# Kernel optimization log

Hardware: AMD Instinct MI355X
Metric: run time of the kernel (lower is better)

## Reference

```python
import jax, jax.numpy as jnp
import numpy as np

EPS = 1e-12  # matches torch F.normalize default eps


def _l2_normalize(x):
    # torch.nn.functional.normalize: x / max(||x||, eps)
    n = jnp.sqrt(jnp.sum(x * x, axis=-1, keepdims=True))
    return x / jnp.maximum(n, EPS)


def setup_inputs() -> dict:
    key = jax.random.key(0)
    kq, kk, kv = jax.random.split(key, 3)
    B, KD, VD, N = 256, 128, 128, 500000
    return {
        "query": jax.random.normal(kq, (B, KD), dtype=jnp.float32),
        "keys": jax.random.normal(kk, (N, KD), dtype=jnp.float32),
        "values": jax.random.normal(kv, (N, VD), dtype=jnp.float32),
        "k": 8,
    }


def reference(query, keys, values, k):
    # Cosine similarity: normalize both sides, dense matmul.
    q_norm = _l2_normalize(query)            # [B, KD]
    k_norm = _l2_normalize(keys)             # [N, KD]
    sim = jnp.matmul(q_norm, k_norm.T)       # [B, N]
    scores, indices = jax.lax.top_k(sim, k)  # [B, k] each
    slots = values[indices]                  # gather -> [B, k, VD]
    return slots, scores
```

## Files before the change

### kernel.cpp

```cpp
#include <hip/hip_runtime.h>
#include <math.h>

#define B     256
#define KD    128
#define VD    128
#define TOPK  8
#define NBK   512
#define QG    4
#define KB    16

typedef __attribute__((ext_vector_type(8))) short bf16x8;
typedef __attribute__((ext_vector_type(4))) float f32x4;

__device__ __forceinline__ bool gt_si(float a, int ai, float b, int bi) {
    return (a > b) || (a == b && ai < bi);
}

__device__ __forceinline__ float bf16lo_f(unsigned int p) { return __uint_as_float(p << 16); }
__device__ __forceinline__ float bf16hi_f(unsigned int p) { return __uint_as_float(p & 0xffff0000u); }

#define SPLIT_PAIR(x0, x1, o1, o2, o3)                                         \
    {                                                                          \
        unsigned int p1_, p2_, p3_;                                            \
        float xx0_ = (x0), xx1_ = (x1);                                        \
        asm("v_cvt_pk_bf16_f32 %0, %1, %2" : "=v"(p1_) : "v"(xx0_), "v"(xx1_));\
        float r0_ = xx0_ - bf16lo_f(p1_);                                      \
        float r1_ = xx1_ - bf16hi_f(p1_);                                      \
        asm("v_cvt_pk_bf16_f32 %0, %1, %2" : "=v"(p2_) : "v"(r0_), "v"(r1_));  \
        float t0_ = r0_ - bf16lo_f(p2_);                                       \
        float t1_ = r1_ - bf16hi_f(p2_);                                       \
        asm("v_cvt_pk_bf16_f32 %0, %1, %2" : "=v"(p3_) : "v"(t0_), "v"(t1_));  \
        o1 = p1_; o2 = p2_; o3 = p3_;                                          \
    }

__global__ __launch_bounds__(64) void k_prep_q(const float* __restrict__ q,
                                               unsigned int* __restrict__ qb) {
    const int qt   = blockIdx.x;
    const int l    = threadIdx.x;
    const int qcol = l & 15;
    const int ck   = l >> 4;
    const int qrow = qt * 16 + qcol;

    const float4* src = (const float4*)(q + (size_t)qrow * KD + ck * 32);
    float4 v[8];
    float ss = 0.f;
#pragma unroll
    for (int i = 0; i < 8; ++i) {
        v[i] = src[i];
        ss += v[i].x * v[i].x + v[i].y * v[i].y + v[i].z * v[i].z + v[i].w * v[i].w;
    }
    ss += __shfl_xor(ss, 16);
    ss += __shfl_xor(ss, 32);
    const float inv = 1.0f / fmaxf(sqrtf(ss), 1e-12f);

    float x[32];
#pragma unroll
    for (int i = 0; i < 8; ++i) {
        x[4 * i + 0] = v[i].x * inv;
        x[4 * i + 1] = v[i].y * inv;
        x[4 * i + 2] = v[i].z * inv;
        x[4 * i + 3] = v[i].w * inv;
    }

#pragma unroll
    for (int h = 0; h < 4; ++h) {
        unsigned int u1[4], u2[4], u3[4];
#pragma unroll
        for (int p = 0; p < 4; ++p) {
            SPLIT_PAIR(x[h * 8 + 2 * p], x[h * 8 + 2 * p + 1], u1[p], u2[p], u3[p]);
        }
        const int lam = h * 16 + qcol;
        *(uint4*)&qb[((((size_t)0 * 16 + qt) * 4 + ck) * 64 + lam) * 4] = make_uint4(u1[0], u1[1], u1[2], u1[3]);
        *(uint4*)&qb[((((size_t)1 * 16 + qt) * 4 + ck) * 64 + lam) * 4] = make_uint4(u2[0], u2[1], u2[2], u2[3]);
        *(uint4*)&qb[((((size_t)2 * 16 + qt) * 4 + ck) * 64 + lam) * 4] = make_uint4(u3[0], u3[1], u3[2], u3[3]);
    }
}

__global__ __launch_bounds__(256, 2) void k_cand(const float* __restrict__ keys,
                                                 const unsigned int* __restrict__ qb,
                                                 float* __restrict__ cand_s,
                                                 int* __restrict__ cand_i,
                                                 int N, int chunk) {
    __shared__ __align__(16) unsigned short lk[3 * 16 * 136];

    const int t  = threadIdx.x;
    const int l  = t & 63;
    const int w  = t >> 6;
    const int bx = blockIdx.x;
    const int qg = blockIdx.y;
    const int qt = qg * 4 + w;

    const int base = bx * chunk;
    const int nend = min(N, base + chunk);

    bf16x8 bq[3][4];
#pragma unroll
    for (int term = 0; term < 3; ++term)
#pragma unroll
        for (int ks = 0; ks < 4; ++ks) {
            const uint4 u = *(const uint4*)&qb[((((size_t)term * 16 + qt) * 4 + ks) * 64 + l) * 4];
            bq[term][ks] = *(const bf16x8*)&u;
        }

    float s[TOPK];
    int   id[TOPK];
#pragma unroll
    for (int j = 0; j < TOPK; ++j) { s[j] = -1e30f; id[j] = 0; }

    const int srow = t >> 4;
    const int sseg = t & 15;
    const int ro   = (l & 15) * 136 + (l >> 4) * 8;

    for (int sb = base; sb < nend; sb += KB) {
        const int row = sb + srow;
        float4 a, c;
        if (row < nend) {
            const float4* kr = (const float4*)(keys + (size_t)row * KD + sseg * 8);
            a = kr[0];
            c = kr[1];
        } else {
            a = make_float4(0.f, 0.f, 0.f, 0.f);
            c = a;
        }
        float ss = a.x * a.x + a.y * a.y + a.z * a.z + a.w * a.w
                 + c.x * c.x + c.y * c.y + c.z * c.z + c.w * c.w;
#pragma unroll
        for (int m = 8; m >= 1; m >>= 1) ss += __shfl_xor(ss, m);
        const float inv = 1.0f / fmaxf(sqrtf(ss), 1e-12f);
        const float x0 = a.x * inv, x1 = a.y * inv, x2 = a.z * inv, x3 = a.w * inv;
        const float x4 = c.x * inv, x5 = c.y * inv, x6 = c.z * inv, x7 = c.w * inv;

        unsigned int u1[4], u2[4], u3[4];
        SPLIT_PAIR(x0, x1, u1[0], u2[0], u3[0]);
        SPLIT_PAIR(x2, x3, u1[1], u2[1], u3[1]);
        SPLIT_PAIR(x4, x5, u1[2], u2[2], u3[2]);
        SPLIT_PAIR(x6, x7, u1[3], u2[3], u3[3]);

        const int wo = srow * 136 + sseg * 8;
        *(uint4*)&lk[0 * 2176 + wo] = make_uint4(u1[0], u1[1], u1[2], u1[3]);
        *(uint4*)&lk[1 * 2176 + wo] = make_uint4(u2[0], u2[1], u2[2], u2[3]);
        *(uint4*)&lk[2 * 2176 + wo] = make_uint4(u3[0], u3[1], u3[2], u3[3]);
        __syncthreads();

        bf16x8 ak[3][4];
#pragma unroll
        for (int term = 0; term < 3; ++term)
#pragma unroll
            for (int ks = 0; ks < 4; ++ks)
                ak[term][ks] = *(const bf16x8*)&lk[term * 2176 + ro + ks * 32];
        __syncthreads();

        f32x4 acc0 = {0.f, 0.f, 0.f, 0.f};
        f32x4 acc1 = {0.f, 0.f, 0.f, 0.f};
        f32x4 acc2 = {0.f, 0.f, 0.f, 0.f};
        f32x4 acc3 = {0.f, 0.f, 0.f, 0.f};
#define PRD(ta, tb)                                                                     \
        acc0 = __builtin_amdgcn_mfma_f32_16x16x32_bf16(ak[ta][0], bq[tb][0], acc0, 0, 0, 0); \
        acc1 = __builtin_amdgcn_mfma_f32_16x16x32_bf16(ak[ta][1], bq[tb][1], acc1, 0, 0, 0); \
        acc2 = __builtin_amdgcn_mfma_f32_16x16x32_bf16(ak[ta][2], bq[tb][2], acc2, 0, 0, 0); \
        acc3 = __builtin_amdgcn_mfma_f32_16x16x32_bf16(ak[ta][3], bq[tb][3], acc3, 0, 0, 0);
        PRD(0, 2) PRD(2, 0) PRD(1, 1) PRD(0, 1) PRD(1, 0) PRD(0, 0)
#undef PRD
        f32x4 sim4 = (acc0 + acc1) + (acc2 + acc3);

        const int kb0 = sb + (l >> 4) * 4;
#pragma unroll
        for (int r = 0; r < 4; ++r) {
            const int kidx = kb0 + r;
            float sim = sim4[r];
            sim = (kidx < nend) ? sim : -1e30f;
            if (sim > s[TOPK - 1]) {
                s[TOPK - 1]  = sim;
                id[TOPK - 1] = kidx;
#pragma unroll
                for (int u = TOPK - 1; u >= 1; --u) {
                    const bool sw = s[u] > s[u - 1];
                    if (sw) {
                        float ts = s[u]; s[u] = s[u - 1]; s[u - 1] = ts;
                        int   ti = id[u]; id[u] = id[u - 1]; id[u - 1] = ti;
                    }
                }
            }
        }
    }

#pragma unroll
    for (int m = 16; m <= 32; m <<= 1) {
        float bs[TOPK]; int bi[TOPK];
#pragma unroll
        for (int j = 0; j < TOPK; ++j) {
            bs[j] = __shfl_xor(s[j], m);
            bi[j] = __shfl_xor(id[j], m);
        }
        float ms[TOPK]; int mi[TOPK];
#pragma unroll
        for (int j = 0; j < TOPK; ++j) {
            const float av = s[j];            const int ai = id[j];
            const float bv = bs[TOPK - 1 - j]; const int b2 = bi[TOPK - 1 - j];
            const bool g = gt_si(av, ai, bv, b2);
            ms[j] = g ? av : bv;
            mi[j] = g ? ai : b2;
        }
#define CAS_(x, y)                                                     \
        { if (!gt_si(ms[x], mi[x], ms[y], mi[y])) {                    \
              float tv = ms[x]; ms[x] = ms[y]; ms[y] = tv;             \
              int   ti = mi[x]; mi[x] = mi[y]; mi[y] = ti; } }
        CAS_(0, 4); CAS_(1, 5); CAS_(2, 6); CAS_(3, 7);
        CAS_(0, 2); CAS_(1, 3); CAS_(4, 6); CAS_(5, 7);
        CAS_(0, 1); CAS_(2, 3); CAS_(4, 5); CAS_(6, 7);
#undef CAS_
#pragma unroll
        for (int j = 0; j < TOPK; ++j) { s[j] = ms[j]; id[j] = mi[j]; }
    }

    if ((l >> 4) == 0) {
        const int q = qt * 16 + (l & 15);
        float* os = cand_s + ((size_t)bx * B + q) * TOPK;
        int*   oi = cand_i + ((size_t)bx * B + q) * TOPK;
#pragma unroll
        for (int j = 0; j < TOPK; ++j) { os[j] = s[j]; oi[j] = id[j]; }
    }
}

__global__ __launch_bounds__(64) void k_merge(const float* __restrict__ cand_s,
                                              const int* __restrict__ cand_i,
                                              const float* __restrict__ values,
                                              float* __restrict__ out_slots,
                                              float* __restrict__ out_scores) {
    const int q    = blockIdx.x;
    const int lane = threadIdx.x;

    float s[TOPK];
    int   id[TOPK];
#pragma unroll
    for (int j = 0; j < TOPK; ++j) { s[j] = -1e30f; id[j] = -1; }

    for (int b = lane; b < NBK; b += 64) {
        const float* cs = cand_s + ((size_t)b * B + q) * TOPK;
        const int*   ci = cand_i + ((size_t)b * B + q) * TOPK;
#pragma unroll
        for (int j = 0; j < TOPK; ++j) {
            const float v  = cs[j];
            const int   vi = ci[j];
            if (gt_si(v, vi, s[TOPK - 1], id[TOPK - 1])) {
                s[TOPK - 1]  = v;
                id[TOPK - 1] = vi;
#pragma unroll
                for (int u = TOPK - 1; u >= 1; --u) {
                    if (gt_si(s[u], id[u], s[u - 1], id[u - 1])) {
                        float ts = s[u]; s[u] = s[u - 1]; s[u - 1] = ts;
                        int   ti = id[u]; id[u] = id[u - 1]; id[u - 1] = ti;
                    }
                }
            }
        }
    }

#pragma unroll
    for (int m = 1; m <= 32; m <<= 1) {
        float bs[TOPK]; int bi[TOPK];
#pragma unroll
        for (int j = 0; j < TOPK; ++j) {
            bs[j] = __shfl_xor(s[j], m);
            bi[j] = __shfl_xor(id[j], m);
        }
        float ms[TOPK]; int mi[TOPK];
#pragma unroll
        for (int j = 0; j < TOPK; ++j) {
            const float av = s[j];            const int ai = id[j];
            const float bv = bs[TOPK - 1 - j]; const int b2 = bi[TOPK - 1 - j];
            const bool g = gt_si(av, ai, bv, b2);
            ms[j] = g ? av : bv;
            mi[j] = g ? ai : b2;
        }
#define CAS_(x, y)                                                     \
        { if (!gt_si(ms[x], mi[x], ms[y], mi[y])) {                    \
              float tv = ms[x]; ms[x] = ms[y]; ms[y] = tv;             \
              int   ti = mi[x]; mi[x] = mi[y]; mi[y] = ti; } }
        CAS_(0, 4); CAS_(1, 5); CAS_(2, 6); CAS_(3, 7);
        CAS_(0, 2); CAS_(1, 3); CAS_(4, 6); CAS_(5, 7);
        CAS_(0, 1); CAS_(2, 3); CAS_(4, 5); CAS_(6, 7);
#undef CAS_
#pragma unroll
        for (int j = 0; j < TOPK; ++j) { s[j] = ms[j]; id[j] = mi[j]; }
    }

    if (lane == 0) {
#pragma unroll
        for (int j = 0; j < TOPK; ++j) out_scores[(size_t)q * TOPK + j] = s[j];
    }

#pragma unroll
    for (int j = 0; j < TOPK; ++j) {
        const int row = id[j];
        const float2* src = (const float2*)(values + (size_t)row * VD);
        float2 v = src[lane];
        ((float2*)(out_slots + ((size_t)q * TOPK + j) * VD))[lane] = v;
    }
}

extern "C" void kernel_launch(void* const* d_in, const int* in_sizes, int n_in,
                              void* d_out, int out_size, void* d_ws, size_t ws_size,
                              hipStream_t stream) {
    const float* q      = (const float*)d_in[0];
    const float* keys   = (const float*)d_in[1];
    const float* values = (const float*)d_in[2];
    const int N = in_sizes[1] / KD;

    float* out_slots  = (float*)d_out;
    float* out_scores = out_slots + (size_t)B * TOPK * VD;

    unsigned int* qbuf = (unsigned int*)d_ws;
    float* cand_s = (float*)(qbuf + 49152);
    int*   cand_i = (int*)(cand_s + (size_t)NBK * B * TOPK);

    const int chunk = (N + NBK - 1) / NBK;

    k_prep_q<<<16, 64, 0, stream>>>(q, qbuf);
    dim3 grid(NBK, QG);
    k_cand<<<grid, 256, 0, stream>>>(keys, qbuf, cand_s, cand_i, N, chunk);
    k_merge<<<B, 64, 0, stream>>>(cand_s, cand_i, values, out_slots, out_scores);
}
```

Measured before the change: 736.8 us.

## Precompute normalized bf16x3 key tiles once and stream them into MFMA

Adds a k_prep_k pass that normalizes every key once and writes its three-term bf16 split, already in the MFMA operand layout, to workspace. The candidate kernel then loads those fragments directly from global memory, with no per-tile normalization, LDS staging or barriers. This removes the conversion work the old kernel repeated for each of the four query groups. Block indices are remapped so the four query groups sharing a key chunk run close together and can reuse it from cache, and the candidate buffer is transposed to query-major for the merge. The cost is writing and rereading a precomputed key buffer about 1.5x the size of the fp32 keys, and the new path needs a large workspace, falling back to the old kernel when it is too small.

```diff
diff --git a/kernel.cpp b/kernel.cpp
--- a/kernel.cpp
+++ b/kernel.cpp
@@ -33,6 +33,11 @@
         o1 = p1_; o2 = p2_; o3 = p3_;                                          \
     }
 
+__device__ __forceinline__ void decode_bq(int flat, int& bx, int& qg) {
+    bx = ((flat >> 5) << 3) | (flat & 7);
+    qg = (flat >> 3) & 3;
+}
+
 __global__ __launch_bounds__(64) void k_prep_q(const float* __restrict__ q,
                                                unsigned int* __restrict__ qb) {
     const int qt   = blockIdx.x;
@@ -76,79 +81,95 @@
     }
 }
 
-__global__ __launch_bounds__(256, 2) void k_cand(const float* __restrict__ keys,
-                                                 const unsigned int* __restrict__ qb,
-                                                 float* __restrict__ cand_s,
-                                                 int* __restrict__ cand_i,
-                                                 int N, int chunk) {
-    __shared__ __align__(16) unsigned short lk[3 * 16 * 136];
-
-    const int t  = threadIdx.x;
-    const int l  = t & 63;
-    const int w  = t >> 6;
-    const int bx = blockIdx.x;
-    const int qg = blockIdx.y;
-    const int qt = qg * 4 + w;
-
-    const int base = bx * chunk;
-    const int nend = min(N, base + chunk);
-
-    bf16x8 bq[3][4];
-#pragma unroll
-    for (int term = 0; term < 3; ++term)
-#pragma unroll
-        for (int ks = 0; ks < 4; ++ks) {
-            const uint4 u = *(const uint4*)&qb[((((size_t)term * 16 + qt) * 4 + ks) * 64 + l) * 4];
-            bq[term][ks] = *(const bf16x8*)&u;
-        }
-
-    float s[TOPK];
-    int   id[TOPK];
-#pragma unroll
-    for (int j = 0; j < TOPK; ++j) { s[j] = -1e30f; id[j] = 0; }
-
-    const int srow = t >> 4;
-    const int sseg = t & 15;
-    const int ro   = (l & 15) * 136 + (l >> 4) * 8;
-
-    for (int sb = base; sb < nend; sb += KB) {
-        const int row = sb + srow;
-        float4 a, c;
-        if (row < nend) {
-            const float4* kr = (const float4*)(keys + (size_t)row * KD + sseg * 8);
-            a = kr[0];
-            c = kr[1];
+__global__ __launch_bounds__(256, 2) void k_prep_k(const float* __restrict__ keys,
+                                                   uint4* __restrict__ kb,
+                                                   int N, int ntiles) {
+    const int w    = threadIdx.x >> 6;
+    const int l    = threadIdx.x & 63;
+    const int tile = blockIdx.x * 4 + w;
+    if (tile >= ntiles) return;
+
+    const int row = tile * 16 + (l & 15);
+    const int h   = l >> 4;
+
+    float4 va[4], vb[4];
+    float ss = 0.f;
+#pragma unroll
+    for (int ks = 0; ks < 4; ++ks) {
+        if (row < N) {
+            const float4* src = (const float4*)(keys + (size_t)row * KD + ks * 32 + h * 8);
+            va[ks] = src[0];
+            vb[ks] = src[1];
         } else {
-            a = make_float4(0.f, 0.f, 0.f, 0.f);
-            c = a;
-        }
-        float ss = a.x * a.x + a.y * a.y + a.z * a.z + a.w * a.w
-                 + c.x * c.x + c.y * c.y + c.z * c.z + c.w * c.w;
-#pragma unroll
-        for (int m = 8; m >= 1; m >>= 1) ss += __shfl_xor(ss, m);
-        const float inv = 1.0f / fmaxf(sqrtf(ss), 1e-12f);
-        const float x0 = a.x * inv, x1 = a.y * inv, x2 = a.z * inv, x3 = a.w * inv;
-        const float x4 = c.x * inv, x5 = c.y * inv, x6 = c.z * inv, x7 = c.w * inv;
-
+            va[ks] = make_float4(0.f, 0.f, 0.f, 0.f);
+            vb[ks] = va[ks];
+        }
+        ss += va[ks].x * va[ks].x + va[ks].y * va[ks].y + va[ks].z * va[ks].z + va[ks].w * va[ks].w
+            + vb[ks].x * vb[ks].x + vb[ks].y * vb[ks].y + vb[ks].z * vb[ks].z + vb[ks].w * vb[ks].w;
+    }
+    ss += __shfl_xor(ss, 16);
+    ss += __shfl_xor(ss, 32);
+    const float inv = 1.0f / fmaxf(sqrtf(ss), 1e-12f);
+
+#pragma unroll
+    for (int ks = 0; ks < 4; ++ks) {
+        const float x0 = va[ks].x * inv, x1 = va[ks].y * inv;
+        const float x2 = va[ks].z * inv, x3 = va[ks].w * inv;
+        const float x4 = vb[ks].x * inv, x5 = vb[ks].y * inv;
+        const float x6 = vb[ks].z * inv, x7 = vb[ks].w * inv;
         unsigned int u1[4], u2[4], u3[4];
         SPLIT_PAIR(x0, x1, u1[0], u2[0], u3[0]);
         SPLIT_PAIR(x2, x3, u1[1], u2[1], u3[1]);
         SPLIT_PAIR(x4, x5, u1[2], u2[2], u3[2]);
         SPLIT_PAIR(x6, x7, u1[3], u2[3], u3[3]);
-
-        const int wo = srow * 136 + sseg * 8;
-        *(uint4*)&lk[0 * 2176 + wo] = make_uint4(u1[0], u1[1], u1[2], u1[3]);
-        *(uint4*)&lk[1 * 2176 + wo] = make_uint4(u2[0], u2[1], u2[2], u2[3]);
-        *(uint4*)&lk[2 * 2176 + wo] = make_uint4(u3[0], u3[1], u3[2], u3[3]);
-        __syncthreads();
-
+        const size_t tb = (size_t)tile * 12;
+        kb[(tb + 0 * 4 + ks) * 64 + l] = make_uint4(u1[0], u1[1], u1[2], u1[3]);
+        kb[(tb + 1 * 4 + ks) * 64 + l] = make_uint4(u2[0], u2[1], u2[2], u2[3]);
+        kb[(tb + 2 * 4 + ks) * 64 + l] = make_uint4(u3[0], u3[1], u3[2], u3[3]);
+    }
+}
+
+__global__ __launch_bounds__(256, 2) void k_cand_fast(const uint4* __restrict__ kb,
+                                                      const unsigned int* __restrict__ qb,
+                                                      float* __restrict__ cand_s,
+                                                      int* __restrict__ cand_i,
+                                                      int N, int ntiles, int tiles_per_bx) {
+    const int t = threadIdx.x;
+    const int l = t & 63;
+    const int w = t >> 6;
+    int bx, qg;
+    decode_bq(blockIdx.x, bx, qg);
+    const int qt = qg * 4 + w;
+
+    const int t0 = bx * tiles_per_bx;
+    const int t1 = min(ntiles, t0 + tiles_per_bx);
+
+    bf16x8 bq[3][4];
+#pragma unroll
+    for (int term = 0; term < 3; ++term)
+#pragma unroll
+        for (int ks = 0; ks < 4; ++ks) {
+            const uint4 u = *(const uint4*)&qb[((((size_t)term * 16 + qt) * 4 + ks) * 64 + l) * 4];
+            bq[term][ks] = *(const bf16x8*)&u;
+        }
+
+    float s[TOPK];
+    int   id[TOPK];
+#pragma unroll
+    for (int j = 0; j < TOPK; ++j) { s[j] = -1e30f; id[j] = 0; }
+
+    const uint4* kbl = kb + l;
+
+    for (int tile = t0; tile < t1; ++tile) {
+        const uint4* kt = kbl + (size_t)tile * 12 * 64;
         bf16x8 ak[3][4];
 #pragma unroll
         for (int term = 0; term < 3; ++term)
 #pragma unroll
-            for (int ks = 0; ks < 4; ++ks)
-                ak[term][ks] = *(const bf16x8*)&lk[term * 2176 + ro + ks * 32];
-        __syncthreads();
+            for (int ks = 0; ks < 4; ++ks) {
+                const uint4 u = kt[(term * 4 + ks) * 64];
+                ak[term][ks] = *(const bf16x8*)&u;
+            }
 
         f32x4 acc0 = {0.f, 0.f, 0.f, 0.f};
         f32x4 acc1 = {0.f, 0.f, 0.f, 0.f};
@@ -163,12 +184,12 @@
 #undef PRD
         f32x4 sim4 = (acc0 + acc1) + (acc2 + acc3);
 
-        const int kb0 = sb + (l >> 4) * 4;
+        const int kb0 = tile * 16 + (l >> 4) * 4;
 #pragma unroll
         for (int r = 0; r < 4; ++r) {
             const int kidx = kb0 + r;
             float sim = sim4[r];
-            sim = (kidx < nend) ? sim : -1e30f;
+            sim = (kidx < N) ? sim : -1e30f;
             if (sim > s[TOPK - 1]) {
                 s[TOPK - 1]  = sim;
                 id[TOPK - 1] = kidx;
@@ -215,39 +236,113 @@
 
     if ((l >> 4) == 0) {
         const int q = qt * 16 + (l & 15);
-        float* os = cand_s + ((size_t)bx * B + q) * TOPK;
-        int*   oi = cand_i + ((size_t)bx * B + q) * TOPK;
+        float* os = cand_s + ((size_t)q * NBK + bx) * TOPK;
+        int*   oi = cand_i + ((size_t)q * NBK + bx) * TOPK;
 #pragma unroll
         for (int j = 0; j < TOPK; ++j) { os[j] = s[j]; oi[j] = id[j]; }
     }
 }
 
-__global__ __launch_bounds__(64) void k_merge(const float* __restrict__ cand_s,
-                                              const int* __restrict__ cand_i,
-                                              const float* __restrict__ values,
-                                              float* __restrict__ out_slots,
-                                              float* __restrict__ out_scores) {
-    const int q    = blockIdx.x;
-    const int lane = threadIdx.x;
+__global__ __launch_bounds__(256, 2) void k_cand_slow(const float* __restrict__ keys,
+                                                      const unsigned int* __restrict__ qb,
+                                                      float* __restrict__ cand_s,
+                                                      int* __restrict__ cand_i,
+                                                      int N, int chunk) {
+    __shared__ __align__(16) unsigned short lk[3 * 16 * 136];
+
+    const int t = threadIdx.x;
+    const int l = t & 63;
+    const int w = t >> 6;
+    int bx, qg;
+    decode_bq(blockIdx.x, bx, qg);
+    const int qt = qg * 4 + w;
+
+    const int base = bx * chunk;
+    const int nend = min(N, base + chunk);
+
+    bf16x8 bq[3][4];
+#pragma unroll
+    for (int term = 0; term < 3; ++term)
+#pragma unroll
+        for (int ks = 0; ks < 4; ++ks) {
+            const uint4 u = *(const uint4*)&qb[((((size_t)term * 16 + qt) * 4 + ks) * 64 + l) * 4];
+            bq[term][ks] = *(const bf16x8*)&u;
+        }
 
     float s[TOPK];
     int   id[TOPK];
 #pragma unroll
-    for (int j = 0; j < TOPK; ++j) { s[j] = -1e30f; id[j] = -1; }
-
-    for (int b = lane; b < NBK; b += 64) {
-        const float* cs = cand_s + ((size_t)b * B + q) * TOPK;
-        const int*   ci = cand_i + ((size_t)b * B + q) * TOPK;
-#pragma unroll
-        for (int j = 0; j < TOPK; ++j) {
-            const float v  = cs[j];
-            const int   vi = ci[j];
-            if (gt_si(v, vi, s[TOPK - 1], id[TOPK - 1])) {
-                s[TOPK - 1]  = v;
-                id[TOPK - 1] = vi;
+    for (int j = 0; j < TOPK; ++j) { s[j] = -1e30f; id[j] = 0; }
+
+    const int srow = t >> 4;
+    const int sseg = t & 15;
+    const int ro   = (l & 15) * 136 + (l >> 4) * 8;
+
+    for (int sb = base; sb < nend; sb += KB) {
+        const int row = sb + srow;
+        float4 a, c;
+        if (row < nend) {
+            const float4* kr = (const float4*)(keys + (size_t)row * KD + sseg * 8);
+            a = kr[0];
+            c = kr[1];
+        } else {
+            a = make_float4(0.f, 0.f, 0.f, 0.f);
+            c = a;
+        }
+        float ss = a.x * a.x + a.y * a.y + a.z * a.z + a.w * a.w
+                 + c.x * c.x + c.y * c.y + c.z * c.z + c.w * c.w;
+#pragma unroll
+        for (int m = 8; m >= 1; m >>= 1) ss += __shfl_xor(ss, m);
+        const float inv = 1.0f / fmaxf(sqrtf(ss), 1e-12f);
+        const float x0 = a.x * inv, x1 = a.y * inv, x2 = a.z * inv, x3 = a.w * inv;
+        const float x4 = c.x * inv, x5 = c.y * inv, x6 = c.z * inv, x7 = c.w * inv;
+
+        unsigned int u1[4], u2[4], u3[4];
+        SPLIT_PAIR(x0, x1, u1[0], u2[0], u3[0]);
+        SPLIT_PAIR(x2, x3, u1[1], u2[1], u3[1]);
+        SPLIT_PAIR(x4, x5, u1[2], u2[2], u3[2]);
+        SPLIT_PAIR(x6, x7, u1[3], u2[3], u3[3]);
+
+        const int wo = srow * 136 + sseg * 8;
+        *(uint4*)&lk[0 * 2176 + wo] = make_uint4(u1[0], u1[1], u1[2], u1[3]);
+        *(uint4*)&lk[1 * 2176 + wo] = make_uint4(u2[0], u2[1], u2[2], u2[3]);
+        *(uint4*)&lk[2 * 2176 + wo] = make_uint4(u3[0], u3[1], u3[2], u3[3]);
+        __syncthreads();
+
+        bf16x8 ak[3][4];
+#pragma unroll
+        for (int term = 0; term < 3; ++term)
+#pragma unroll
+            for (int ks = 0; ks < 4; ++ks)
+                ak[term][ks] = *(const bf16x8*)&lk[term * 2176 + ro + ks * 32];
+        __syncthreads();
+
+        f32x4 acc0 = {0.f, 0.f, 0.f, 0.f};
+        f32x4 acc1 = {0.f, 0.f, 0.f, 0.f};
+        f32x4 acc2 = {0.f, 0.f, 0.f, 0.f};
+        f32x4 acc3 = {0.f, 0.f, 0.f, 0.f};
+#define PRD(ta, tb)                                                                     \
+        acc0 = __builtin_amdgcn_mfma_f32_16x16x32_bf16(ak[ta][0], bq[tb][0], acc0, 0, 0, 0); \
+        acc1 = __builtin_amdgcn_mfma_f32_16x16x32_bf16(ak[ta][1], bq[tb][1], acc1, 0, 0, 0); \
+        acc2 = __builtin_amdgcn_mfma_f32_16x16x32_bf16(ak[ta][2], bq[tb][2], acc2, 0, 0, 0); \
+        acc3 = __builtin_amdgcn_mfma_f32_16x16x32_bf16(ak[ta][3], bq[tb][3], acc3, 0, 0, 0);
+        PRD(0, 2) PRD(2, 0) PRD(1, 1) PRD(0, 1) PRD(1, 0) PRD(0, 0)
+#undef PRD
+        f32x4 sim4 = (acc0 + acc1) + (acc2 + acc3);
+
+        const int kb0 = sb + (l >> 4) * 4;
+#pragma unroll
+        for (int r = 0; r < 4; ++r) {
+            const int kidx = kb0 + r;
+            float sim = sim4[r];
+            sim = (kidx < nend) ? sim : -1e30f;
+            if (sim > s[TOPK - 1]) {
+                s[TOPK - 1]  = sim;
+                id[TOPK - 1] = kidx;
 #pragma unroll
                 for (int u = TOPK - 1; u >= 1; --u) {
-                    if (gt_si(s[u], id[u], s[u - 1], id[u - 1])) {
+                    const bool sw = s[u] > s[u - 1];
+                    if (sw) {
                         float ts = s[u]; s[u] = s[u - 1]; s[u - 1] = ts;
                         int   ti = id[u]; id[u] = id[u - 1]; id[u - 1] = ti;
                     }
@@ -257,7 +352,7 @@
     }
 
 #pragma unroll
-    for (int m = 1; m <= 32; m <<= 1) {
+    for (int m = 16; m <= 32; m <<= 1) {
         float bs[TOPK]; int bi[TOPK];
 #pragma unroll
         for (int j = 0; j < TOPK; ++j) {
@@ -285,6 +380,78 @@
         for (int j = 0; j < TOPK; ++j) { s[j] = ms[j]; id[j] = mi[j]; }
     }
 
+    if ((l >> 4) == 0) {
+        const int q = qt * 16 + (l & 15);
+        float* os = cand_s + ((size_t)q * NBK + bx) * TOPK;
+        int*   oi = cand_i + ((size_t)q * NBK + bx) * TOPK;
+#pragma unroll
+        for (int j = 0; j < TOPK; ++j) { os[j] = s[j]; oi[j] = id[j]; }
+    }
+}
+
+__global__ __launch_bounds__(64) void k_merge(const float* __restrict__ cand_s,
+                                              const int* __restrict__ cand_i,
+                                              const float* __restrict__ values,
+                                              float* __restrict__ out_slots,
+                                              float* __restrict__ out_scores) {
+    const int q    = blockIdx.x;
+    const int lane = threadIdx.x;
+
+    float s[TOPK];
+    int   id[TOPK];
+#pragma unroll
+    for (int j = 0; j < TOPK; ++j) { s[j] = -1e30f; id[j] = -1; }
+
+    for (int b = lane; b < NBK; b += 64) {
+        const float* cs = cand_s + ((size_t)q * NBK + b) * TOPK;
+        const int*   ci = cand_i + ((size_t)q * NBK + b) * TOPK;
+#pragma unroll
+        for (int j = 0; j < TOPK; ++j) {
+            const float v  = cs[j];
+            const int   vi = ci[j];
+            if (gt_si(v, vi, s[TOPK - 1], id[TOPK - 1])) {
+                s[TOPK - 1]  = v;
+                id[TOPK - 1] = vi;
+#pragma unroll
+                for (int u = TOPK - 1; u >= 1; --u) {
+                    if (gt_si(s[u], id[u], s[u - 1], id[u - 1])) {
+                        float ts = s[u]; s[u] = s[u - 1]; s[u - 1] = ts;
+                        int   ti = id[u]; id[u] = id[u - 1]; id[u - 1] = ti;
+                    }
+                }
+            }
+        }
+    }
+
+#pragma unroll
+    for (int m = 1; m <= 32; m <<= 1) {
+        float bs[TOPK]; int bi[TOPK];
+#pragma unroll
+        for (int j = 0; j < TOPK; ++j) {
+            bs[j] = __shfl_xor(s[j], m);
+            bi[j] = __shfl_xor(id[j], m);
+        }
+        float ms[TOPK]; int mi[TOPK];
+#pragma unroll
+        for (int j = 0; j < TOPK; ++j) {
+            const float av = s[j];            const int ai = id[j];
+            const float bv = bs[TOPK - 1 - j]; const int b2 = bi[TOPK - 1 - j];
+            const bool g = gt_si(av, ai, bv, b2);
+            ms[j] = g ? av : bv;
+            mi[j] = g ? ai : b2;
+        }
+#define CAS_(x, y)                                                     \
+        { if (!gt_si(ms[x], mi[x], ms[y], mi[y])) {                    \
+              float tv = ms[x]; ms[x] = ms[y]; ms[y] = tv;             \
+              int   ti = mi[x]; mi[x] = mi[y]; mi[y] = ti; } }
+        CAS_(0, 4); CAS_(1, 5); CAS_(2, 6); CAS_(3, 7);
+        CAS_(0, 2); CAS_(1, 3); CAS_(4, 6); CAS_(5, 7);
+        CAS_(0, 1); CAS_(2, 3); CAS_(4, 5); CAS_(6, 7);
+#undef CAS_
+#pragma unroll
+        for (int j = 0; j < TOPK; ++j) { s[j] = ms[j]; id[j] = mi[j]; }
+    }
+
     if (lane == 0) {
 #pragma unroll
         for (int j = 0; j < TOPK; ++j) out_scores[(size_t)q * TOPK + j] = s[j];
@@ -312,12 +479,23 @@
 
     unsigned int* qbuf = (unsigned int*)d_ws;
     float* cand_s = (float*)(qbuf + 49152);
-    int*   cand_i = (int*)(cand_s + (size_t)NBK * B * TOPK);
-
-    const int chunk = (N + NBK - 1) / NBK;
+    int*   cand_i = (int*)(cand_s + (size_t)B * NBK * TOPK);
+    uint4* kb     = (uint4*)(cand_i + (size_t)B * NBK * TOPK);
+
+    const int ntiles       = (N + 15) >> 4;
+    const int tiles_per_bx = (ntiles + NBK - 1) / NBK;
+    const size_t kb_off  = 196608 + 2 * (size_t)B * NBK * TOPK * 4;
+    const size_t need    = kb_off + (size_t)ntiles * 12 * 64 * 16;
 
     k_prep_q<<<16, 64, 0, stream>>>(q, qbuf);
-    dim3 grid(NBK, QG);
-    k_cand<<<grid, 256, 0, stream>>>(keys, qbuf, cand_s, cand_i, N, chunk);
+
+    if (ws_size >= need) {
+        k_prep_k<<<(ntiles + 3) / 4, 256, 0, stream>>>(keys, kb, N, ntiles);
+        k_cand_fast<<<NBK * QG, 256, 0, stream>>>(kb, qbuf, cand_s, cand_i,
+                                                  N, ntiles, tiles_per_bx);
+    } else {
+        const int chunk = (N + NBK - 1) / NBK;
+        k_cand_slow<<<NBK * QG, 256, 0, stream>>>(keys, qbuf, cand_s, cand_i, N, chunk);
+    }
     k_merge<<<B, 64, 0, stream>>>(cand_s, cand_i, values, out_slots, out_scores);
 }
```

Result: slower. 851.2 us (+15.5%).
